# Optimization experiments

Hardware: AMD Instinct MI355X
Metric: run time of the kernel (lower is better)

Reference implementation:

```python
import jax, jax.numpy as jnp
import numpy as np

B, N, D = 8, 4096, 3


def setup_inputs() -> dict:
    key = jax.random.key(0)
    k1, k2 = jax.random.split(key)
    array1 = jax.random.normal(k1, (B, N, D), dtype=jnp.float32)
    array2 = jax.random.normal(k2, (B, N, D), dtype=jnp.float32)
    return {"array1": array1, "array2": array2}


def reference(array1, array2):
    # Pairwise squared distances: sq[b, i, j] = ||array1[b,i] - array2[b,j]||^2
    diff = array1[:, :, None, :] - array2[:, None, :, :]   # [B, N1, N2, D]
    sq = jnp.sum(diff * diff, axis=-1)                     # [B, N1, N2]
    # array2samples_distance(a1, a2): for each point of a2, min dist to a1, then mean
    av_dist1 = jnp.mean(jnp.min(sq, axis=1), axis=-1)      # [B] (min over array1 points)
    # array2samples_distance(a2, a1): for each point of a1, min dist to a2, then mean
    av_dist2 = jnp.mean(jnp.min(sq, axis=2), axis=-1)      # [B] (min over array2 points)
    dist1 = jnp.mean(av_dist1)
    dist2 = jnp.mean(av_dist2)
    dist_all = dist1 + dist2
    return (dist_all, dist1, dist2)
```

## Files before the change

kernel.cpp:

```cpp
#include <hip/hip_runtime.h>

#define BB 8
#define NN 4096
#define THREADS 256
#define NSPLIT 64
#define CHUNK (NN / NSPLIT)
#define NPAIR (CHUNK / 2)
#define QPT 16
#define NQ (BB * NN)
#define NQ_TOTAL (2 * NQ)

typedef float v2f __attribute__((ext_vector_type(2)));

template <int SEL>
__device__ __forceinline__ v2f pk3(v2f X2, v2f Y2, v2f Z2, v2f W2,
                                   v2f qx, v2f qy, v2f qz) {
    v2f t;
    if constexpr (SEL == 0) {
        asm("v_pk_fma_f32 %0, %1, %2, %3 op_sel:[0,0,0] op_sel_hi:[1,0,1]"
            : "=v"(t) : "v"(Z2), "v"(qz), "v"(W2));
        asm("v_pk_fma_f32 %0, %1, %2, %0 op_sel:[0,0,0] op_sel_hi:[1,0,1]"
            : "+v"(t) : "v"(Y2), "v"(qy));
        asm("v_pk_fma_f32 %0, %1, %2, %0 op_sel:[0,0,0] op_sel_hi:[1,0,1]"
            : "+v"(t) : "v"(X2), "v"(qx));
    } else {
        asm("v_pk_fma_f32 %0, %1, %2, %3 op_sel:[0,1,0] op_sel_hi:[1,1,1]"
            : "=v"(t) : "v"(Z2), "v"(qz), "v"(W2));
        asm("v_pk_fma_f32 %0, %1, %2, %0 op_sel:[0,1,0] op_sel_hi:[1,1,1]"
            : "+v"(t) : "v"(Y2), "v"(qy));
        asm("v_pk_fma_f32 %0, %1, %2, %0 op_sel:[0,1,0] op_sel_hi:[1,1,1]"
            : "+v"(t) : "v"(X2), "v"(qx));
    }
    return t;
}

__global__ __launch_bounds__(THREADS) void chamfer_min_kernel(
    const float* __restrict__ a1, const float* __restrict__ a2,
    float* __restrict__ minpart)
{
    __shared__ float4 sdb4[2 * NPAIR];

    const int tid = threadIdx.x;
    const int bid = blockIdx.x;
    const int c   = bid & (NSPLIT - 1);
    const int b   = (bid >> 6) & 7;
    const int dir = bid >> 9;

    const float* dbg = (dir == 0 ? a1 : a2) + (size_t)b * NN * 3;
    const float* qg  = (dir == 0 ? a2 : a1) + (size_t)b * NN * 3;

    if (tid < NPAIR) {
        const float2* s2 = reinterpret_cast<const float2*>(dbg + (size_t)c * CHUNK * 3);
        const float2 u = s2[3 * tid + 0];
        const float2 v = s2[3 * tid + 1];
        const float2 w = s2[3 * tid + 2];
        const float w0 = 0.5f * fmaf(u.x, u.x, fmaf(u.y, u.y, v.x * v.x));
        const float w1 = 0.5f * fmaf(v.y, v.y, fmaf(w.x, w.x, w.y * w.y));
        sdb4[2 * tid]     = make_float4(u.x, v.y, u.y, w.x);
        sdb4[2 * tid + 1] = make_float4(v.x, w.y, w0, w1);
    }

    v2f qc[3][QPT / 2];
    {
        const float4* q4 = reinterpret_cast<const float4*>(qg + (size_t)tid * QPT * 3);
        float f[48];
        #pragma unroll
        for (int v = 0; v < 12; ++v) {
            const float4 w = q4[v];
            f[4 * v + 0] = w.x; f[4 * v + 1] = w.y;
            f[4 * v + 2] = w.z; f[4 * v + 3] = w.w;
        }
        #pragma unroll
        for (int k2 = 0; k2 < QPT / 2; ++k2) {
            qc[0][k2] = (v2f){-f[6 * k2 + 0], -f[6 * k2 + 3]};
            qc[1][k2] = (v2f){-f[6 * k2 + 1], -f[6 * k2 + 4]};
            qc[2][k2] = (v2f){-f[6 * k2 + 2], -f[6 * k2 + 5]};
        }
    }

    __syncthreads();

    float m[QPT];
    #pragma unroll
    for (int k = 0; k < QPT; ++k) m[k] = 3.4e38f;

    #pragma unroll 2
    for (int ip = 0; ip < NPAIR; ++ip) {
        const float4 A  = sdb4[2 * ip];
        const float4 Bv = sdb4[2 * ip + 1];
        const v2f X2 = (v2f){A.x,  A.y};
        const v2f Y2 = (v2f){A.z,  A.w};
        const v2f Z2 = (v2f){Bv.x, Bv.y};
        const v2f W2 = (v2f){Bv.z, Bv.w};
        #pragma unroll
        for (int k2 = 0; k2 < QPT / 2; ++k2) {
            const v2f t0 = pk3<0>(X2, Y2, Z2, W2, qc[0][k2], qc[1][k2], qc[2][k2]);
            m[2 * k2]     = fminf(fminf(t0[0], t0[1]), m[2 * k2]);
            const v2f t1 = pk3<1>(X2, Y2, Z2, W2, qc[0][k2], qc[1][k2], qc[2][k2]);
            m[2 * k2 + 1] = fminf(fminf(t1[0], t1[1]), m[2 * k2 + 1]);
        }
    }

    const size_t qglob = (size_t)dir * NQ + (size_t)b * NN + (size_t)tid * QPT;
    float4* dst = reinterpret_cast<float4*>(minpart + (size_t)c * NQ_TOTAL + qglob);
    #pragma unroll
    for (int v = 0; v < 4; ++v)
        dst[v] = make_float4(m[4 * v], m[4 * v + 1], m[4 * v + 2], m[4 * v + 3]);
}

__global__ __launch_bounds__(THREADS) void decode_sum_kernel(
    const float* __restrict__ a1, const float* __restrict__ a2,
    const float* __restrict__ minpart, float* __restrict__ partials)
{
    __shared__ float red[THREADS];
    const int tid = threadIdx.x;
    const int bid = blockIdx.x;
    const int gq  = bid * THREADS + tid;
    const int dir = gq >> 15;
    const int b   = (gq >> 12) & 7;
    const int q   = gq & (NN - 1);

    float mn = 3.4e38f;
    #pragma unroll
    for (int cc = 0; cc < NSPLIT; ++cc)
        mn = fminf(mn, minpart[(size_t)cc * NQ_TOTAL + gq]);

    const float* qp = (dir == 0 ? a2 : a1) + ((size_t)b * NN + q) * 3;
    const float qx = qp[0], qy = qp[1], qz = qp[2];
    const float qn = fmaf(qx, qx, fmaf(qy, qy, qz * qz));
    const float d  = fmaf(2.0f, mn, qn);

    red[tid] = d;
    __syncthreads();
    #pragma unroll
    for (int s = THREADS / 2; s > 0; s >>= 1) {
        if (tid < s) red[tid] += red[tid + s];
        __syncthreads();
    }
    if (tid == 0) partials[bid] = red[0];
}

__global__ __launch_bounds__(256) void finalize_kernel(
    const float* __restrict__ partials, float* __restrict__ out)
{
    __shared__ float red[256];
    const int t = threadIdx.x;
    red[t] = partials[t];
    __syncthreads();
    #pragma unroll
    for (int s = 64; s > 0; s >>= 1) {
        if ((t & 127) < s) red[t] += red[t + s];
        __syncthreads();
    }
    if (t == 0) {
        const float inv = 1.0f / (float)(BB * NN);
        const float d1 = red[0]   * inv;
        const float d2 = red[128] * inv;
        out[0] = d1 + d2;
        out[1] = d1;
        out[2] = d2;
    }
}

extern "C" void kernel_launch(void* const* d_in, const int* in_sizes, int n_in,
                              void* d_out, int out_size, void* d_ws, size_t ws_size,
                              hipStream_t stream)
{
    const float* a1 = (const float*)d_in[0];
    const float* a2 = (const float*)d_in[1];
    float* out = (float*)d_out;

    float* minpart  = (float*)d_ws;
    float* partials = (float*)((char*)d_ws + (size_t)NSPLIT * NQ_TOTAL * sizeof(float));

    hipLaunchKernelGGL(chamfer_min_kernel, dim3(2 * BB * NSPLIT), dim3(THREADS), 0, stream,
                       a1, a2, minpart);
    hipLaunchKernelGGL(decode_sum_kernel, dim3(NQ_TOTAL / THREADS), dim3(THREADS), 0, stream,
                       a1, a2, minpart, partials);
    hipLaunchKernelGGL(finalize_kernel, dim3(1), dim3(256), 0, stream,
                       partials, out);
}
```

Baseline: 40.10 us.

## Cut DB split count, halve queries per thread, prefetch LDS pairs

The database-split factor drops from 64 to 16. Each block now covers a 256-point database chunk against half of a batch's queries, with 8 queries per thread instead of 16. This is meant to shrink the intermediate partial-min buffer fourfold, which cuts both the global writes in the main kernel and the reads in the decode kernel, and to lower register pressure. The inner loop is also hand-unrolled by two pairs and software-prefetches the next two shared-memory pairs. The trade-off is more LDS reads per FMA, since each broadcast point now serves fewer queries.

```diff
diff --git a/kernel.cpp b/kernel.cpp
--- a/kernel.cpp
+++ b/kernel.cpp
@@ -3,10 +3,11 @@
 #define BB 8
 #define NN 4096
 #define THREADS 256
-#define NSPLIT 64
+#define NSPLIT 16
 #define CHUNK (NN / NSPLIT)
 #define NPAIR (CHUNK / 2)
-#define QPT 16
+#define QPT 8
+#define QPB (THREADS * QPT)
 #define NQ (BB * NN)
 #define NQ_TOTAL (2 * NQ)
 
@@ -43,8 +44,9 @@
     const int tid = threadIdx.x;
     const int bid = blockIdx.x;
     const int c   = bid & (NSPLIT - 1);
-    const int b   = (bid >> 6) & 7;
-    const int dir = bid >> 9;
+    const int qb  = (bid >> 4) & 1;
+    const int b   = (bid >> 5) & 7;
+    const int dir = bid >> 8;
 
     const float* dbg = (dir == 0 ? a1 : a2) + (size_t)b * NN * 3;
     const float* qg  = (dir == 0 ? a2 : a1) + (size_t)b * NN * 3;
@@ -60,52 +62,78 @@
         sdb4[2 * tid + 1] = make_float4(v.x, w.y, w0, w1);
     }
 
-    v2f qc[3][QPT / 2];
+    v2f qc0[QPT / 2], qc1[QPT / 2], qc2[QPT / 2];
     {
-        const float4* q4 = reinterpret_cast<const float4*>(qg + (size_t)tid * QPT * 3);
-        float f[48];
-        #pragma unroll
-        for (int v = 0; v < 12; ++v) {
-            const float4 w = q4[v];
-            f[4 * v + 0] = w.x; f[4 * v + 1] = w.y;
-            f[4 * v + 2] = w.z; f[4 * v + 3] = w.w;
+        const float4* q4 = reinterpret_cast<const float4*>(
+            qg + (size_t)(qb * QPB + tid * QPT) * 3);
+        const float4 v0 = q4[0], v1 = q4[1], v2 = q4[2];
+        const float4 v3 = q4[3], v4 = q4[4], v5 = q4[5];
+        qc0[0] = (v2f){-v0.x, -v0.w};  qc1[0] = (v2f){-v0.y, -v1.x};  qc2[0] = (v2f){-v0.z, -v1.y};
+        qc0[1] = (v2f){-v1.z, -v2.y};  qc1[1] = (v2f){-v1.w, -v2.z};  qc2[1] = (v2f){-v2.x, -v2.w};
+        qc0[2] = (v2f){-v3.x, -v3.w};  qc1[2] = (v2f){-v3.y, -v4.x};  qc2[2] = (v2f){-v3.z, -v4.y};
+        qc0[3] = (v2f){-v4.z, -v5.y};  qc1[3] = (v2f){-v4.w, -v5.z};  qc2[3] = (v2f){-v5.x, -v5.w};
+    }
+
+    __syncthreads();
+
+    float m[QPT];
+    #pragma unroll
+    for (int k = 0; k < QPT; ++k) m[k] = 3.4e38f;
+
+    float4 A0 = sdb4[0], B0 = sdb4[1];
+    float4 A1 = sdb4[2], B1 = sdb4[3];
+    for (int ip = 0; ip < NPAIR - 2; ip += 2) {
+        const float4 nA0 = sdb4[2 * ip + 4];
+        const float4 nB0 = sdb4[2 * ip + 5];
+        const float4 nA1 = sdb4[2 * ip + 6];
+        const float4 nB1 = sdb4[2 * ip + 7];
+        {
+            const v2f X2 = (v2f){A0.x, A0.y}, Y2 = (v2f){A0.z, A0.w};
+            const v2f Z2 = (v2f){B0.x, B0.y}, W2 = (v2f){B0.z, B0.w};
+            #pragma unroll
+            for (int k2 = 0; k2 < QPT / 2; ++k2) {
+                const v2f t0 = pk3<0>(X2, Y2, Z2, W2, qc0[k2], qc1[k2], qc2[k2]);
+                m[2 * k2]     = fminf(fminf(t0[0], t0[1]), m[2 * k2]);
+                const v2f t1 = pk3<1>(X2, Y2, Z2, W2, qc0[k2], qc1[k2], qc2[k2]);
+                m[2 * k2 + 1] = fminf(fminf(t1[0], t1[1]), m[2 * k2 + 1]);
+            }
         }
+        {
+            const v2f X2 = (v2f){A1.x, A1.y}, Y2 = (v2f){A1.z, A1.w};
+            const v2f Z2 = (v2f){B1.x, B1.y}, W2 = (v2f){B1.z, B1.w};
+            #pragma unroll
+            for (int k2 = 0; k2 < QPT / 2; ++k2) {
+                const v2f t0 = pk3<0>(X2, Y2, Z2, W2, qc0[k2], qc1[k2], qc2[k2]);
+                m[2 * k2]     = fminf(fminf(t0[0], t0[1]), m[2 * k2]);
+                const v2f t1 = pk3<1>(X2, Y2, Z2, W2, qc0[k2], qc1[k2], qc2[k2]);
+                m[2 * k2 + 1] = fminf(fminf(t1[0], t1[1]), m[2 * k2 + 1]);
+            }
+        }
+        A0 = nA0; B0 = nB0; A1 = nA1; B1 = nB1;
+    }
+    #pragma unroll
+    for (int rep = 0; rep < 2; ++rep) {
+        const float4 A = rep ? A1 : A0;
+        const float4 Bv = rep ? B1 : B0;
+        const v2f X2 = (v2f){A.x, A.y}, Y2 = (v2f){A.z, A.w};
+        const v2f Z2 = (v2f){Bv.x, Bv.y}, W2 = (v2f){Bv.z, Bv.w};
         #pragma unroll
         for (int k2 = 0; k2 < QPT / 2; ++k2) {
-            qc[0][k2] = (v2f){-f[6 * k2 + 0], -f[6 * k2 + 3]};
-            qc[1][k2] = (v2f){-f[6 * k2 + 1], -f[6 * k2 + 4]};
-            qc[2][k2] = (v2f){-f[6 * k2 + 2], -f[6 * k2 + 5]};
-        }
-    }
-
-    __syncthreads();
-
-    float m[QPT];
-    #pragma unroll
-    for (int k = 0; k < QPT; ++k) m[k] = 3.4e38f;
-
-    #pragma unroll 2
-    for (int ip = 0; ip < NPAIR; ++ip) {
-        const float4 A  = sdb4[2 * ip];
-        const float4 Bv = sdb4[2 * ip + 1];
-        const v2f X2 = (v2f){A.x,  A.y};
-        const v2f Y2 = (v2f){A.z,  A.w};
-        const v2f Z2 = (v2f){Bv.x, Bv.y};
-        const v2f W2 = (v2f){Bv.z, Bv.w};
-        #pragma unroll
-        for (int k2 = 0; k2 < QPT / 2; ++k2) {
-            const v2f t0 = pk3<0>(X2, Y2, Z2, W2, qc[0][k2], qc[1][k2], qc[2][k2]);
+            const v2f t0 = pk3<0>(X2, Y2, Z2, W2, qc0[k2], qc1[k2], qc2[k2]);
             m[2 * k2]     = fminf(fminf(t0[0], t0[1]), m[2 * k2]);
-            const v2f t1 = pk3<1>(X2, Y2, Z2, W2, qc[0][k2], qc[1][k2], qc[2][k2]);
+            const v2f t1 = pk3<1>(X2, Y2, Z2, W2, qc0[k2], qc1[k2], qc2[k2]);
             m[2 * k2 + 1] = fminf(fminf(t1[0], t1[1]), m[2 * k2 + 1]);
         }
     }
 
-    const size_t qglob = (size_t)dir * NQ + (size_t)b * NN + (size_t)tid * QPT;
+    float4 o0, o1;
+    o0.x = m[0]; o0.y = m[1]; o0.z = m[2]; o0.w = m[3];
+    o1.x = m[4]; o1.y = m[5]; o1.z = m[6]; o1.w = m[7];
+
+    const size_t qglob = (size_t)dir * NQ + (size_t)b * NN + (size_t)(qb * QPB + tid * QPT);
     float4* dst = reinterpret_cast<float4*>(minpart + (size_t)c * NQ_TOTAL + qglob);
-    #pragma unroll
-    for (int v = 0; v < 4; ++v)
-        dst[v] = make_float4(m[4 * v], m[4 * v + 1], m[4 * v + 2], m[4 * v + 3]);
+    dst[0] = o0;
+    dst[1] = o1;
 }
 
 __global__ __launch_bounds__(THREADS) void decode_sum_kernel(
@@ -173,7 +201,7 @@
     float* minpart  = (float*)d_ws;
     float* partials = (float*)((char*)d_ws + (size_t)NSPLIT * NQ_TOTAL * sizeof(float));
 
-    hipLaunchKernelGGL(chamfer_min_kernel, dim3(2 * BB * NSPLIT), dim3(THREADS), 0, stream,
+    hipLaunchKernelGGL(chamfer_min_kernel, dim3(2 * BB * 2 * NSPLIT), dim3(THREADS), 0, stream,
                        a1, a2, minpart);
     hipLaunchKernelGGL(decode_sum_kernel, dim3(NQ_TOTAL / THREADS), dim3(THREADS), 0, stream,
                        a1, a2, minpart, partials);
```

Result: faster. 33.19 us (-17.2%).
